# Kernel optimization log

Hardware: AMD Instinct MI355X
Metric: run time of the kernel (lower is better)

Reference implementation:

```python
import jax, jax.numpy as jnp
import numpy as np

B, N, F_IN, F_OUT = 128, 512, 128, 64
ALPHA = 0.2        # LeakyReLU slope for attention logits
GAIN = 1.414       # xavier gain used in the torch module
NEG_INF = -9e15    # mask value from the torch code


def _xavier_uniform(key, shape, gain):
    fan_in, fan_out = shape[0], shape[1]
    limit = gain * np.sqrt(6.0 / (fan_in + fan_out))
    return jax.random.uniform(key, shape, jnp.float32, -limit, limit)


def setup_inputs() -> dict:
    key = jax.random.key(0)
    k1, k2, k3, k4 = jax.random.split(key, 4)
    input_hid = jax.random.normal(k1, (B, N, F_IN), jnp.float32)
    adj = jax.random.randint(k2, (B, N, N), 0, 2, jnp.int32)  # 0/1 adjacency
    W = _xavier_uniform(k3, (F_IN, F_OUT), GAIN)
    a = _xavier_uniform(k4, (2 * F_OUT, 1), GAIN)
    return {"input_hid": input_hid, "adj": adj, "W": W, "a": a}


def reference(input_hid, adj, W, a):
    # h: [B, N, F_OUT]
    h = jnp.matmul(input_hid, W)
    # Standard GAT decomposition of the concat-repeat construction:
    # e[b,i,j] = leakyrelu( [h_i || h_j] @ a ) = leakyrelu( h_i@a_src + h_j@a_dst )
    a_src = a[:F_OUT, 0]   # applies to the repeated-row (i) half
    a_dst = a[F_OUT:, 0]   # applies to the tiled (j) half
    s = jnp.einsum('bnf,f->bn', h, a_src)  # [B, N]
    t = jnp.einsum('bnf,f->bn', h, a_dst)  # [B, N]
    e = jax.nn.leaky_relu(s[:, :, None] + t[:, None, :], ALPHA)  # [B, N, N]
    e = jnp.where(adj > 0, e, NEG_INF)
    att = jax.nn.softmax(e, axis=2)        # softmax over neighbors j
    h_prime = jnp.matmul(att, h)           # [B, N, F_OUT]
    # concat=True -> F.leaky_relu with torch default slope 0.01
    return jax.nn.leaky_relu(h_prime, 0.01)
```

## Files before the change

### kernel.cpp

```cpp
#include <hip/hip_runtime.h>
#include <stdint.h>

#define B_   128
#define N_   512
#define FIN  128
#define FOUT 64

using bf16x8 = __attribute__((ext_vector_type(8))) short;
using f32x4  = __attribute__((ext_vector_type(4))) float;

__device__ inline unsigned short f2bf(float x) {
    union { float f; uint32_t u; } c; c.f = x;
    uint32_t u = c.u;
    return (unsigned short)((u + 0x7FFFu + ((u >> 16) & 1u)) >> 16);
}

__global__ __launch_bounds__(256) void k_h(const float* __restrict__ X,
                                           const float* __restrict__ W,
                                           const float* __restrict__ a,
                                           uint16_t* __restrict__ htT,
                                           float* __restrict__ s,
                                           float* __restrict__ t) {
    __shared__ bf16x8 wl[16 * 64];

    const int b  = blockIdx.x >> 2;
    const int j0 = (blockIdx.x & 3) * 128;
    const int tid = threadIdx.x;
    const int w = tid >> 6, lane = tid & 63;
    const int q = lane >> 4, m = lane & 15;

#pragma unroll
    for (int nt = 0; nt < 4; ++nt) {
        bf16x8 fr;
#pragma unroll
        for (int u = 0; u < 8; ++u)
            fr[u] = (short)f2bf(W[(w * 32 + q * 8 + u) * FOUT + nt * 16 + m]);
        wl[(w * 4 + nt) * 64 + lane] = fr;
    }
    __syncthreads();

    float asv[4], adv[4];
#pragma unroll
    for (int nt = 0; nt < 4; ++nt) {
        asv[nt] = a[nt * 16 + m];
        adv[nt] = a[FOUT + nt * 16 + m];
    }

    const float* xb = X + ((size_t)(b * N_) + j0) * FIN;

    for (int rl = 0; rl < 2; ++rl) {
        const int rt = w + rl * 4;
        const float* xrow = xb + (size_t)(rt * 16 + m) * FIN + q * 8;
        f32x4 acc[4] = {{0.f,0.f,0.f,0.f},{0.f,0.f,0.f,0.f},
                        {0.f,0.f,0.f,0.f},{0.f,0.f,0.f,0.f}};
#pragma unroll
        for (int ks = 0; ks < 4; ++ks) {
            float4 v0 = *(const float4*)(xrow + ks * 32);
            float4 v1 = *(const float4*)(xrow + ks * 32 + 4);
            bf16x8 af;
            af[0] = (short)f2bf(v0.x); af[1] = (short)f2bf(v0.y);
            af[2] = (short)f2bf(v0.z); af[3] = (short)f2bf(v0.w);
            af[4] = (short)f2bf(v1.x); af[5] = (short)f2bf(v1.y);
            af[6] = (short)f2bf(v1.z); af[7] = (short)f2bf(v1.w);
#pragma unroll
            for (int nt = 0; nt < 4; ++nt)
                acc[nt] = __builtin_amdgcn_mfma_f32_16x16x32_bf16(
                    af, wl[(ks * 4 + nt) * 64 + lane], acc[nt], 0, 0, 0);
        }

        float ps[4], pt[4];
#pragma unroll
        for (int r = 0; r < 4; ++r) {
            float vs = 0.f, vt = 0.f;
#pragma unroll
            for (int nt = 0; nt < 4; ++nt) {
                vs += acc[nt][r] * asv[nt];
                vt += acc[nt][r] * adv[nt];
            }
            vs += __shfl_xor(vs, 1, 64); vs += __shfl_xor(vs, 2, 64);
            vs += __shfl_xor(vs, 4, 64); vs += __shfl_xor(vs, 8, 64);
            vt += __shfl_xor(vt, 1, 64); vt += __shfl_xor(vt, 2, 64);
            vt += __shfl_xor(vt, 4, 64); vt += __shfl_xor(vt, 8, 64);
            ps[r] = vs; pt[r] = vt;
        }
        if (m < 4) {
            float vs = (m == 0) ? ps[0] : (m == 1) ? ps[1] : (m == 2) ? ps[2] : ps[3];
            float vt = (m == 0) ? pt[0] : (m == 1) ? pt[1] : (m == 2) ? pt[2] : pt[3];
            int row = j0 + rt * 16 + q * 4 + m;
            s[b * N_ + row] = vs;
            t[b * N_ + row] = vt;
        }

#pragma unroll
        for (int nt = 0; nt < 4; ++nt) {
            uint32_t d0 = (uint32_t)f2bf(acc[nt][0]) | ((uint32_t)f2bf(acc[nt][1]) << 16);
            uint32_t d1 = (uint32_t)f2bf(acc[nt][2]) | ((uint32_t)f2bf(acc[nt][3]) << 16);
            uint2 dd; dd.x = d0; dd.y = d1;
            *(uint2*)(htT + (size_t)(b * FOUT + nt * 16 + m) * N_ + j0 + rt * 16 + q * 4) = dd;
        }
    }
}

__global__ __launch_bounds__(512, 4) void k_attn(const int*    __restrict__ adj,
                                                 const uint16_t* __restrict__ htT,
                                                 const float*  __restrict__ s,
                                                 const float*  __restrict__ t,
                                                 float*        __restrict__ out) {
    __shared__ bf16x8 hstage[64 * 64];
    __shared__ float  tsh[N_];

    const int b  = blockIdx.x >> 2;
    const int i0 = (blockIdx.x & 3) * 128;
    const int tid = threadIdx.x;
    const int w = tid >> 6, lane = tid & 63;
    const int q = lane >> 4, m = lane & 15;

    const uint16_t* hb = htT + (size_t)b * FOUT * N_;

#pragma unroll
    for (int i = 0; i < 8; ++i) {
        int pi = i * 8 + w, ks = pi >> 2, nt = pi & 3;
        hstage[pi * 64 + lane] =
            *(const bf16x8*)(hb + (size_t)(nt * 16 + m) * N_ + ks * 32 + q * 8);
    }
    tsh[tid] = t[b * N_ + tid];
    __syncthreads();

    const int irow = i0 + w * 16 + m;
    const float s_i = s[b * N_ + irow];
    const int* ar = adj + ((size_t)(b * N_) + irow) * N_;

    f32x4 acc[4] = {{0.f,0.f,0.f,0.f},{0.f,0.f,0.f,0.f},
                    {0.f,0.f,0.f,0.f},{0.f,0.f,0.f,0.f}};
    float lsum = 0.f;

    int4 qa[4], qb[4];
#pragma unroll
    for (int d = 0; d < 4; ++d) {
        qa[d] = *(const int4*)(ar + d * 32 + q * 8);
        qb[d] = *(const int4*)(ar + d * 32 + q * 8 + 4);
    }

#pragma unroll 4
    for (int ks = 0; ks < 16; ++ks) {
        const int slot = ks & 3;
        int4 c0 = qa[slot];
        int4 c1 = qb[slot];

        const int kp = (ks + 4 < 16) ? ks + 4 : 15;
        qa[slot] = *(const int4*)(ar + kp * 32 + q * 8);
        qb[slot] = *(const int4*)(ar + kp * 32 + q * 8 + 4);

        const int jb = ks * 32 + q * 8;
        float4 tj0 = *(const float4*)&tsh[jb];
        float4 tj1 = *(const float4*)&tsh[jb + 4];
        float tj[8] = {tj0.x, tj0.y, tj0.z, tj0.w, tj1.x, tj1.y, tj1.z, tj1.w};

        int av[8] = {c0.x, c0.y, c0.z, c0.w, c1.x, c1.y, c1.z, c1.w};
        bf16x8 af;
#pragma unroll
        for (int u = 0; u < 8; ++u) {
            float e = s_i + tj[u];
            e = fmaxf(e, 0.2f * e);
            float p = (av[u] > 0) ? __expf(e) : 0.0f;
            lsum += p;
            af[u] = (short)f2bf(p);
        }

        bf16x8 bf0 = hstage[(ks * 4 + 0) * 64 + lane];
        bf16x8 bf1 = hstage[(ks * 4 + 1) * 64 + lane];
        bf16x8 bf2 = hstage[(ks * 4 + 2) * 64 + lane];
        bf16x8 bf3 = hstage[(ks * 4 + 3) * 64 + lane];

        acc[0] = __builtin_amdgcn_mfma_f32_16x16x32_bf16(af, bf0, acc[0], 0, 0, 0);
        acc[1] = __builtin_amdgcn_mfma_f32_16x16x32_bf16(af, bf1, acc[1], 0, 0, 0);
        acc[2] = __builtin_amdgcn_mfma_f32_16x16x32_bf16(af, bf2, acc[2], 0, 0, 0);
        acc[3] = __builtin_amdgcn_mfma_f32_16x16x32_bf16(af, bf3, acc[3], 0, 0, 0);
    }

    lsum += __shfl_xor(lsum, 16, 64);
    lsum += __shfl_xor(lsum, 32, 64);

#pragma unroll
    for (int reg = 0; reg < 4; ++reg) {
        float lr = __shfl(lsum, q * 4 + reg, 64);
        float inv = 1.0f / lr;
        int orow = i0 + w * 16 + q * 4 + reg;
        size_t ob = ((size_t)(b * N_) + orow) * FOUT + m;
#pragma unroll
        for (int nt = 0; nt < 4; ++nt) {
            float v = acc[nt][reg] * inv;
            v = fmaxf(v, 0.01f * v);
            out[ob + nt * 16] = v;
        }
    }
}

extern "C" void kernel_launch(void* const* d_in, const int* in_sizes, int n_in,
                              void* d_out, int out_size, void* d_ws, size_t ws_size,
                              hipStream_t stream) {
    const float* X   = (const float*)d_in[0];
    const int*   adj = (const int*)  d_in[1];
    const float* W   = (const float*)d_in[2];
    const float* a   = (const float*)d_in[3];
    float* out = (float*)d_out;

    uint16_t* htT = (uint16_t*)d_ws;
    float* s = (float*)(htT + (size_t)B_ * FOUT * N_);
    float* t = s + B_ * N_;

    k_h<<<B_ * 4, 256, 0, stream>>>(X, W, a, htT, s, t);
    k_attn<<<B_ * 4, 512, 0, stream>>>(adj, htT, s, t, out);
}
```

Before: 235.2 us.

## Stage adjacency as bitmask in LDS with coalesced ballot loads; reorder block mapping

Each wave now reads its 16 adjacency rows with fully coalesced 64-lane loads, packs them into bitmasks via ballot, and stores the masks in shared memory. The inner loop tests mask bits instead of holding per-lane int4 prefetch registers. Block index mapping also changes so consecutive blocks cover different batches. The goal is better coalescing of the dominant 128 MB adjacency read and lower register pressure. The cost is that the adjacency load now happens as a serialized prologue before compute, with no overlap against the main loop.

```diff
diff --git a/kernel.cpp b/kernel.cpp
--- a/kernel.cpp
+++ b/kernel.cpp
@@ -106,16 +106,33 @@
                                                  const float*  __restrict__ s,
                                                  const float*  __restrict__ t,
                                                  float*        __restrict__ out) {
-    __shared__ bf16x8 hstage[64 * 64];
-    __shared__ float  tsh[N_];
-
-    const int b  = blockIdx.x >> 2;
-    const int i0 = (blockIdx.x & 3) * 128;
+    __shared__ bf16x8   hstage[64 * 64];
+    __shared__ uint32_t lmask[128 * 18];
+    __shared__ float    tsh[N_];
+
+    const int bi = blockIdx.x;
+    const int b  = bi & 127;
+    const int i0 = (bi >> 7) * 128;
     const int tid = threadIdx.x;
     const int w = tid >> 6, lane = tid & 63;
     const int q = lane >> 4, m = lane & 15;
 
     const uint16_t* hb = htT + (size_t)b * FOUT * N_;
+
+    const int* arow_base = adj + ((size_t)(b * N_) + i0) * N_;
+#pragma unroll 2
+    for (int r = 0; r < 16; ++r) {
+        const int row = w * 16 + r;
+        const int* ap = arow_base + (size_t)row * N_;
+#pragma unroll
+        for (int it = 0; it < 8; ++it) {
+            unsigned long long mb = __ballot(ap[it * 64 + lane] > 0);
+            if (lane == 0) {
+                lmask[row * 18 + it * 2]     = (uint32_t)mb;
+                lmask[row * 18 + it * 2 + 1] = (uint32_t)(mb >> 32);
+            }
+        }
+    }
 
 #pragma unroll
     for (int i = 0; i < 8; ++i) {
@@ -128,41 +145,28 @@
 
     const int irow = i0 + w * 16 + m;
     const float s_i = s[b * N_ + irow];
-    const int* ar = adj + ((size_t)(b * N_) + irow) * N_;
+    const uint32_t* mymask = &lmask[(w * 16 + m) * 18];
 
     f32x4 acc[4] = {{0.f,0.f,0.f,0.f},{0.f,0.f,0.f,0.f},
                     {0.f,0.f,0.f,0.f},{0.f,0.f,0.f,0.f}};
     float lsum = 0.f;
 
-    int4 qa[4], qb[4];
-#pragma unroll
-    for (int d = 0; d < 4; ++d) {
-        qa[d] = *(const int4*)(ar + d * 32 + q * 8);
-        qb[d] = *(const int4*)(ar + d * 32 + q * 8 + 4);
-    }
-
-#pragma unroll 4
+#pragma unroll
     for (int ks = 0; ks < 16; ++ks) {
-        const int slot = ks & 3;
-        int4 c0 = qa[slot];
-        int4 c1 = qb[slot];
-
-        const int kp = (ks + 4 < 16) ? ks + 4 : 15;
-        qa[slot] = *(const int4*)(ar + kp * 32 + q * 8);
-        qb[slot] = *(const int4*)(ar + kp * 32 + q * 8 + 4);
+        const uint32_t word = mymask[ks];
+        const uint32_t bm = (word >> (q * 8)) & 0xffu;
 
         const int jb = ks * 32 + q * 8;
         float4 tj0 = *(const float4*)&tsh[jb];
         float4 tj1 = *(const float4*)&tsh[jb + 4];
         float tj[8] = {tj0.x, tj0.y, tj0.z, tj0.w, tj1.x, tj1.y, tj1.z, tj1.w};
 
-        int av[8] = {c0.x, c0.y, c0.z, c0.w, c1.x, c1.y, c1.z, c1.w};
         bf16x8 af;
 #pragma unroll
         for (int u = 0; u < 8; ++u) {
             float e = s_i + tj[u];
             e = fmaxf(e, 0.2f * e);
-            float p = (av[u] > 0) ? __expf(e) : 0.0f;
+            float p = (bm & (1u << u)) ? __expf(e) : 0.0f;
             lsum += p;
             af[u] = (short)f2bf(p);
         }
```

New measurement: 282.4 us. 20.1% more time.
